# Optimization experiments

Measured on AMD Instinct MI355X. Metric: run time of the kernel, lower is better.

## Reference

```python
import jax, jax.numpy as jnp
import numpy as np

B, N, D = 8, 2048, 512
S = 4096  # max_swaps


def setup_inputs() -> dict:
    key = jax.random.key(0)
    ks = jax.random.split(key, 5)
    h = jax.random.normal(ks[0], (B, N, D), dtype=jnp.float32)
    indices = jax.random.randint(ks[1], (B, S, 4), 0, N, dtype=jnp.int64)
    # MLP params (Linear stores weight as (out,in) in torch; we keep (in,out) and matmul)
    W1 = jax.random.normal(ks[2], (4 * D, D), dtype=jnp.float32) * (1.0 / np.sqrt(4 * D))
    b1 = jnp.zeros((D,), dtype=jnp.float32)
    W2 = jax.random.normal(ks[3], (D, D // 2), dtype=jnp.float32) * (1.0 / np.sqrt(D))
    b2 = jnp.zeros((D // 2,), dtype=jnp.float32)
    W3 = jax.random.normal(ks[4], (D // 2, 1), dtype=jnp.float32) * (1.0 / np.sqrt(D // 2))
    b3 = jnp.zeros((1,), dtype=jnp.float32)
    return {"h": h, "indices": indices, "W1": W1, "b1": b1, "W2": W2, "b2": b2, "W3": W3, "b3": b3}


def reference(h, indices, W1, b1, W2, b2, W3, b3):
    # h: (B, N, D); indices: (B, S, 4) node ids per swap
    swap_emb = jnp.take_along_axis(h[:, None, :, :], indices[..., None].astype(jnp.int32),
                                   axis=2)  # broadcast-gather -> (B, S, 4, D)
    # equivalently: h[batch_idx, indices]; implemented as per-batch gather
    swap_emb = jax.vmap(lambda hb, ib: hb[ib])(h, indices)  # (B, S, 4, D)
    swap_feats = swap_emb.reshape(h.shape[0], indices.shape[1], -1)  # (B, S, 4D)
    x = jax.nn.gelu(swap_feats @ W1 + b1, approximate=False)
    x = jax.nn.gelu(x @ W2 + b2, approximate=False)
    scores = (x @ W3 + b3)[..., 0]  # (B, S)
    rates = jax.nn.softplus(scores)
    return rates
```

## Files before the change

### kernel.cpp

```cpp
#include <hip/hip_runtime.h>
#include <math.h>

#define BATCH 8
#define NNODES 2048
#define DDIM 512
#define SWAPS 4096
#define M_TOTAL (BATCH * SWAPS)
#define KD DDIM
#define K2 DDIM
#define N2 (DDIM / 2)

typedef __attribute__((ext_vector_type(8))) __bf16 bf16x8;
typedef __attribute__((ext_vector_type(4))) float f32x4;
typedef __attribute__((ext_vector_type(8))) unsigned short us8;
typedef unsigned short ushort_t;

__device__ __forceinline__ float gelu_fast(float x) {
    const float u = 0.7978845608028654f * x * fmaf(0.044715f * x, x, 1.0f);
    const float e = __expf(-2.0f * fabsf(u));
    float t = (1.0f - e) / (1.0f + e);
    t = copysignf(t, u);
    return 0.5f * x * (1.0f + t);
}
__device__ __forceinline__ float softplus_f(float x) {
    return fmaxf(x, 0.0f) + log1pf(expf(-fabsf(x)));
}
__device__ __forceinline__ unsigned short f2bf(float f) {
    unsigned int u = __builtin_bit_cast(unsigned int, f);
    u += 0x7FFFu + ((u >> 16) & 1u);
    return (unsigned short)(u >> 16);
}
__device__ __forceinline__ float bf2f(unsigned short s) {
    return __builtin_bit_cast(float, (unsigned int)s << 16);
}
__device__ __forceinline__ void glds16(const void* g, void* l) {
    __builtin_amdgcn_global_load_lds(
        (const __attribute__((address_space(1))) void*)g,
        (__attribute__((address_space(3))) void*)l, 16, 0, 0);
}

__global__ __launch_bounds__(256) void convert_kernel(
    const float* __restrict__ h, const float* __restrict__ W1,
    const float* __restrict__ W2, ushort_t* __restrict__ h_bf,
    ushort_t* __restrict__ W1pt, ushort_t* __restrict__ W2f)
{
    const int bid = blockIdx.x;
    if (bid < 8192) {
        size_t i = ((size_t)bid * 256 + threadIdx.x) * 4;
        float4 v = *(const float4*)(h + i);
        ushort4 o = { f2bf(v.x), f2bf(v.y), f2bf(v.z), f2bf(v.w) };
        *(ushort4*)(h_bf + i) = o;
    } else if (bid < 8192 + 1024) {
        size_t e = ((size_t)(bid - 8192) * 256 + threadIdx.x) * 4;
        const int k = (int)(e >> 9), n = (int)(e & 511);
        const int sg = k >> 9, d = k & 511;
        const int j = sg * 512 + n;
        float4 v = *(const float4*)(W1 + e);
        W1pt[(size_t)(j + 0) * KD + d] = f2bf(v.x);
        W1pt[(size_t)(j + 1) * KD + d] = f2bf(v.y);
        W1pt[(size_t)(j + 2) * KD + d] = f2bf(v.z);
        W1pt[(size_t)(j + 3) * KD + d] = f2bf(v.w);
    } else {
        size_t e = ((size_t)(bid - 9216) * 256 + threadIdx.x) * 4;
        const int k = (int)(e >> 8), n = (int)(e & 255);
        const int kc = k >> 5, quad = (k >> 3) & 3, pos = k & 7;
        const size_t base = (size_t)kc * 8192 + quad * 8 + pos;
        float4 v = *(const float4*)(W2 + e);
        W2f[base + (size_t)(n + 0) * 32] = f2bf(v.x);
        W2f[base + (size_t)(n + 1) * 32] = f2bf(v.y);
        W2f[base + (size_t)(n + 2) * 32] = f2bf(v.z);
        W2f[base + (size_t)(n + 3) * 32] = f2bf(v.w);
    }
}

__global__ __launch_bounds__(256) void gemm1_dense(
    const ushort_t* __restrict__ h_bf, const ushort_t* __restrict__ W1pt,
    ushort_t* __restrict__ P2)
{
    __shared__ __align__(16) char smem[32768];

    const int tid = threadIdx.x;
    const int w = tid >> 6, lane = tid & 63;
    const int quad = lane >> 4, l16 = lane & 15;
    const int wr = w >> 1, wc = w & 1;

    const int bid = blockIdx.x;
    const int xcd = bid & 7;
    const int r = bid >> 3;
    const int m0 = xcd * NNODES + (r & 15) * 128;
    const int n0 = (r >> 4) * 128;

    const int row0 = tid >> 2, sub = tid & 3;
    const int cg = (sub - (row0 >> 1)) & 3;
    const ushort_t* bA0 = h_bf + (size_t)(m0 + row0) * KD + cg * 8;
    const ushort_t* bA1 = h_bf + (size_t)(m0 + row0 + 64) * KD + cg * 8;
    const ushort_t* bB0 = W1pt + (size_t)(n0 + row0) * KD + cg * 8;
    const ushort_t* bB1 = W1pt + (size_t)(n0 + row0 + 64) * KD + cg * 8;

    int pa[4], pb[4];
    #pragma unroll
    for (int i = 0; i < 4; ++i) {
        const int rA = wr * 64 + i * 16 + l16;
        const int rB = wc * 64 + i * 16 + l16;
        pa[i] = rA * 64 + (((quad + (rA >> 1)) & 3) * 16);
        pb[i] = 8192 + rB * 64 + (((quad + (rB >> 1)) & 3) * 16);
    }

    f32x4 acc[4][4] = {};

    auto stage = [&](int kt, int half) {
        const int oo = kt * 32;
        char* base = smem + half * 16384;
        glds16(bA0 + oo, base + w * 1024);
        glds16(bA1 + oo, base + 4096 + w * 1024);
        glds16(bB0 + oo, base + 8192 + w * 1024);
        glds16(bB1 + oo, base + 12288 + w * 1024);
    };
    auto compute = [&](int half) {
        const char* base = smem + half * 16384;
        bf16x8 af[4], bfr[4];
        #pragma unroll
        for (int i = 0; i < 4; ++i) {
            af[i]  = *(const bf16x8*)(base + pa[i]);
            bfr[i] = *(const bf16x8*)(base + pb[i]);
        }
        #pragma unroll
        for (int i = 0; i < 4; ++i)
            #pragma unroll
            for (int jj = 0; jj < 4; ++jj)
                acc[i][jj] = __builtin_amdgcn_mfma_f32_16x16x32_bf16(
                    af[i], bfr[jj], acc[i][jj], 0, 0, 0);
    };

    for (int kt = 0; kt < 16; kt += 2) {
        stage(kt, 0);
        stage(kt + 1, 1);
        __syncthreads();
        compute(0);
        compute(1);
        __syncthreads();
    }

    #pragma unroll
    for (int jj = 0; jj < 4; ++jj) {
        const int j = n0 + wc * 64 + jj * 16 + l16;
        const int sg = j >> 9, nh = j & 511;
        const size_t base = ((size_t)(xcd * 2 + (nh >> 8)) * NNODES) * 1024
                          + (size_t)(sg << 8) + (nh & 255);
        #pragma unroll
        for (int i = 0; i < 4; ++i) {
            f32x4 v = acc[i][jj];
            #pragma unroll
            for (int rr = 0; rr < 4; ++rr) {
                const int node = (m0 + wr * 64 + i * 16 + quad * 4 + rr) & (NNODES - 1);
                P2[base + (size_t)node * 1024] = f2bf(v[rr]);
            }
        }
    }
}

__global__ __launch_bounds__(512) void fused_tail(
    const ushort_t* __restrict__ P2, const int* __restrict__ idx,
    const float* __restrict__ b1, const ushort_t* __restrict__ W2f,
    const float* __restrict__ b2, const float* __restrict__ W3,
    const float* __restrict__ b3, float* __restrict__ out)
{
    __shared__ __align__(16) char smem[66560];

    const int tid = threadIdx.x;
    const int w = tid >> 6, lane = tid & 63;
    const int quad = lane >> 4, l16 = lane & 15;

    const int bid = blockIdx.x;
    const int b = bid & 7;
    const int m0 = b * SWAPS + (bid >> 3) * 64;

    {
        const int row = tid >> 3;
        const int ws  = tid & 7;
        const int ap  = ws & 3;
        const int ncs = ws >> 2;
        const int acg = (ap - (row >> 1)) & 3;
        const int4 iv = *(const int4*)(idx + (size_t)(m0 + row) * 4);
        const ushort_t* Pr = P2 + (size_t)(b * 2 + ncs) * NNODES * 1024;
        const ushort_t* p0 = Pr + (size_t)iv.x * 1024 + 0 * 256;
        const ushort_t* p1 = Pr + (size_t)iv.y * 1024 + 1 * 256;
        const ushort_t* p2 = Pr + (size_t)iv.z * 1024 + 2 * 256;
        const ushort_t* p3 = Pr + (size_t)iv.w * 1024 + 3 * 256;
        #pragma unroll 4
        for (int it = 0; it < 8; ++it) {
            const int kc = ncs * 8 + it;
            const int pos0 = it * 32 + acg * 8;
            us8 v0 = *(const us8*)(p0 + pos0);
            us8 v1 = *(const us8*)(p1 + pos0);
            us8 v2 = *(const us8*)(p2 + pos0);
            us8 v3 = *(const us8*)(p3 + pos0);
            const float* bp = b1 + ncs * 256 + pos0;
            float4 ba = *(const float4*)bp;
            float4 bb = *(const float4*)(bp + 4);
            float s[8] = { ba.x, ba.y, ba.z, ba.w, bb.x, bb.y, bb.z, bb.w };
            #pragma unroll
            for (int e = 0; e < 8; ++e)
                s[e] += bf2f(v0[e]) + bf2f(v1[e]) + bf2f(v2[e]) + bf2f(v3[e]);
            us8 o;
            #pragma unroll
            for (int e = 0; e < 8; ++e) o[e] = f2bf(gelu_fast(s[e]));
            *(us8*)(smem + kc * 4096 + row * 64 + ap * 16) = o;
        }
    }
    __syncthreads();

    const int rg = w >> 2, cg = w & 3;
    int paRow[2];
    #pragma unroll
    for (int i = 0; i < 2; ++i) {
        const int rA = rg * 32 + i * 16 + l16;
        paRow[i] = rA * 64 + (((quad + (rA >> 1)) & 3) * 16);
    }
    const ushort_t* Bbase = W2f + (size_t)(cg * 64 + l16) * 32 + quad * 8;

    f32x4 acc[2][4] = {};

    #pragma unroll 2
    for (int kc = 0; kc < 16; ++kc) {
        bf16x8 af0 = *(const bf16x8*)(smem + kc * 4096 + paRow[0]);
        bf16x8 af1 = *(const bf16x8*)(smem + kc * 4096 + paRow[1]);
        #pragma unroll
        for (int jf = 0; jf < 4; ++jf) {
            bf16x8 bfr = *(const bf16x8*)(Bbase + (size_t)kc * 8192 + jf * 512);
            acc[0][jf] = __builtin_amdgcn_mfma_f32_16x16x32_bf16(af0, bfr, acc[0][jf], 0, 0, 0);
            acc[1][jf] = __builtin_amdgcn_mfma_f32_16x16x32_bf16(af1, bfr, acc[1][jf], 0, 0, 0);
        }
    }

    float part[2][4] = {};
    #pragma unroll
    for (int jf = 0; jf < 4; ++jf) {
        const int n = cg * 64 + jf * 16 + l16;
        const float w3 = W3[n];
        const float bb2 = b2[n];
        #pragma unroll
        for (int i = 0; i < 2; ++i) {
            f32x4 v = acc[i][jf];
            #pragma unroll
            for (int rr = 0; rr < 4; ++rr)
                part[i][rr] = fmaf(gelu_fast(v[rr] + bb2), w3, part[i][rr]);
        }
    }
    #pragma unroll
    for (int off = 1; off < 16; off <<= 1)
        #pragma unroll
        for (int i = 0; i < 2; ++i)
            #pragma unroll
            for (int rr = 0; rr < 4; ++rr)
                part[i][rr] += __shfl_xor(part[i][rr], off);

    float* red = (float*)(smem + 65536);
    if (l16 == 0) {
        #pragma unroll
        for (int i = 0; i < 2; ++i)
            #pragma unroll
            for (int rr = 0; rr < 4; ++rr)
                red[cg * 64 + rg * 32 + i * 16 + quad * 4 + rr] = part[i][rr];
    }
    __syncthreads();
    if (tid < 64) {
        const float v = red[tid] + red[64 + tid] + red[128 + tid] + red[192 + tid];
        out[m0 + tid] = softplus_f(v + b3[0]);
    }
}

extern "C" void kernel_launch(void* const* d_in, const int* in_sizes, int n_in,
                              void* d_out, int out_size, void* d_ws, size_t ws_size,
                              hipStream_t stream) {
    const float* h   = (const float*)d_in[0];
    const int*   idx = (const int*)d_in[1];
    const float* W1  = (const float*)d_in[2];
    const float* b1  = (const float*)d_in[3];
    const float* W2  = (const float*)d_in[4];
    const float* b2  = (const float*)d_in[5];
    const float* W3  = (const float*)d_in[6];
    const float* b3  = (const float*)d_in[7];
    float* out = (float*)d_out;

    char* ws = (char*)d_ws;
    ushort_t* P2    = (ushort_t*)ws;
    ushort_t* h_bf  = (ushort_t*)(ws + (64u << 20));
    ushort_t* W1pt  = (ushort_t*)(ws + (80u << 20));
    ushort_t* W2f   = (ushort_t*)(ws + (82u << 20));

    convert_kernel<<<9344, 256, 0, stream>>>(h, W1, W2, h_bf, W1pt, W2f);
    gemm1_dense<<<2048, 256, 0, stream>>>(h_bf, W1pt, P2);
    fused_tail<<<512, 512, 0, stream>>>(P2, idx, b1, W2f, b2, W3, b3, out);
}
```

Measured before the change: 179.2 us.

## Widen gemm1 tile to 128x256 and transpose W1 through LDS tiles

The dense gemm1 kernel now computes a 128x256 output tile per block instead of 128x128. Each wave holds 4x8 accumulators, and B fragments are reused across the four A rows, which halves the grid and cuts how often the h_bf tiles are reloaded. Separately, the W1 convert path now transposes through a padded shared-memory tile and writes 16-byte vectors instead of scattered 2-byte stores. The trade-off is more registers and LDS per block (48KB), which lowers occupancy, and fewer blocks (1024) to fill the GPU.

```diff
diff --git a/kernel.cpp b/kernel.cpp
--- a/kernel.cpp
+++ b/kernel.cpp
@@ -45,23 +45,40 @@
     ushort_t* __restrict__ W1pt, ushort_t* __restrict__ W2f)
 {
     const int bid = blockIdx.x;
+    const int tid = threadIdx.x;
     if (bid < 8192) {
-        size_t i = ((size_t)bid * 256 + threadIdx.x) * 4;
+        size_t i = ((size_t)bid * 256 + tid) * 4;
         float4 v = *(const float4*)(h + i);
         ushort4 o = { f2bf(v.x), f2bf(v.y), f2bf(v.z), f2bf(v.w) };
         *(ushort4*)(h_bf + i) = o;
-    } else if (bid < 8192 + 1024) {
-        size_t e = ((size_t)(bid - 8192) * 256 + threadIdx.x) * 4;
-        const int k = (int)(e >> 9), n = (int)(e & 511);
-        const int sg = k >> 9, d = k & 511;
-        const int j = sg * 512 + n;
-        float4 v = *(const float4*)(W1 + e);
-        W1pt[(size_t)(j + 0) * KD + d] = f2bf(v.x);
-        W1pt[(size_t)(j + 1) * KD + d] = f2bf(v.y);
-        W1pt[(size_t)(j + 2) * KD + d] = f2bf(v.z);
-        W1pt[(size_t)(j + 3) * KD + d] = f2bf(v.w);
+    } else if (bid < 8192 + 256) {
+        __shared__ ushort_t sT[64][72];
+        const int tb = bid - 8192;
+        const int kt = tb >> 3, nt = tb & 7;
+        const int kl = tid >> 4;
+        const int n4 = (tid & 15) * 4;
+        #pragma unroll
+        for (int p = 0; p < 4; ++p) {
+            const int k_local = p * 16 + kl;
+            float4 v = *(const float4*)(W1 + (size_t)(kt * 64 + k_local) * 512
+                                        + nt * 64 + n4);
+            sT[n4 + 0][k_local] = f2bf(v.x);
+            sT[n4 + 1][k_local] = f2bf(v.y);
+            sT[n4 + 2][k_local] = f2bf(v.z);
+            sT[n4 + 3][k_local] = f2bf(v.w);
+        }
+        __syncthreads();
+        const int n_local = tid >> 2, ch = tid & 3;
+        const int j = (kt >> 3) * 512 + nt * 64 + n_local;
+        const int d0 = (kt & 7) * 64 + ch * 16;
+        us8 o0, o1;
+        #pragma unroll
+        for (int e = 0; e < 8; ++e) { o0[e] = sT[n_local][ch * 16 + e];
+                                      o1[e] = sT[n_local][ch * 16 + 8 + e]; }
+        *(us8*)(W1pt + (size_t)j * KD + d0)     = o0;
+        *(us8*)(W1pt + (size_t)j * KD + d0 + 8) = o1;
     } else {
-        size_t e = ((size_t)(bid - 9216) * 256 + threadIdx.x) * 4;
+        size_t e = ((size_t)(bid - 8448) * 256 + tid) * 4;
         const int k = (int)(e >> 8), n = (int)(e & 255);
         const int kc = k >> 5, quad = (k >> 3) & 3, pos = k & 7;
         const size_t base = (size_t)kc * 8192 + quad * 8 + pos;
@@ -77,7 +94,7 @@
     const ushort_t* __restrict__ h_bf, const ushort_t* __restrict__ W1pt,
     ushort_t* __restrict__ P2)
 {
-    __shared__ __align__(16) char smem[32768];
+    __shared__ __align__(16) char smem[49152];
 
     const int tid = threadIdx.x;
     const int w = tid >> 6, lane = tid & 63;
@@ -88,48 +105,54 @@
     const int xcd = bid & 7;
     const int r = bid >> 3;
     const int m0 = xcd * NNODES + (r & 15) * 128;
-    const int n0 = (r >> 4) * 128;
+    const int n0 = (r >> 4) * 256;
 
     const int row0 = tid >> 2, sub = tid & 3;
     const int cg = (sub - (row0 >> 1)) & 3;
     const ushort_t* bA0 = h_bf + (size_t)(m0 + row0) * KD + cg * 8;
     const ushort_t* bA1 = h_bf + (size_t)(m0 + row0 + 64) * KD + cg * 8;
-    const ushort_t* bB0 = W1pt + (size_t)(n0 + row0) * KD + cg * 8;
-    const ushort_t* bB1 = W1pt + (size_t)(n0 + row0 + 64) * KD + cg * 8;
-
-    int pa[4], pb[4];
+    const ushort_t* bB[4];
+    #pragma unroll
+    for (int g = 0; g < 4; ++g)
+        bB[g] = W1pt + (size_t)(n0 + g * 64 + row0) * KD + cg * 8;
+
+    int pa[4], pb[8];
     #pragma unroll
     for (int i = 0; i < 4; ++i) {
         const int rA = wr * 64 + i * 16 + l16;
-        const int rB = wc * 64 + i * 16 + l16;
         pa[i] = rA * 64 + (((quad + (rA >> 1)) & 3) * 16);
-        pb[i] = 8192 + rB * 64 + (((quad + (rB >> 1)) & 3) * 16);
-    }
-
-    f32x4 acc[4][4] = {};
+    }
+    #pragma unroll
+    for (int jf = 0; jf < 8; ++jf) {
+        const int rB = wc * 128 + jf * 16 + l16;
+        pb[jf] = 8192 + rB * 64 + (((quad + (rB >> 1)) & 3) * 16);
+    }
+
+    f32x4 acc[4][8] = {};
 
     auto stage = [&](int kt, int half) {
         const int oo = kt * 32;
-        char* base = smem + half * 16384;
+        char* base = smem + half * 24576;
         glds16(bA0 + oo, base + w * 1024);
         glds16(bA1 + oo, base + 4096 + w * 1024);
-        glds16(bB0 + oo, base + 8192 + w * 1024);
-        glds16(bB1 + oo, base + 12288 + w * 1024);
+        #pragma unroll
+        for (int g = 0; g < 4; ++g)
+            glds16(bB[g] + oo, base + 8192 + g * 4096 + w * 1024);
     };
     auto compute = [&](int half) {
-        const char* base = smem + half * 16384;
-        bf16x8 af[4], bfr[4];
+        const char* base = smem + half * 24576;
+        bf16x8 bfr[8];
+        #pragma unroll
+        for (int jf = 0; jf < 8; ++jf)
+            bfr[jf] = *(const bf16x8*)(base + pb[jf]);
         #pragma unroll
         for (int i = 0; i < 4; ++i) {
-            af[i]  = *(const bf16x8*)(base + pa[i]);
-            bfr[i] = *(const bf16x8*)(base + pb[i]);
-        }
-        #pragma unroll
-        for (int i = 0; i < 4; ++i)
-            #pragma unroll
-            for (int jj = 0; jj < 4; ++jj)
-                acc[i][jj] = __builtin_amdgcn_mfma_f32_16x16x32_bf16(
-                    af[i], bfr[jj], acc[i][jj], 0, 0, 0);
+            bf16x8 af = *(const bf16x8*)(base + pa[i]);
+            #pragma unroll
+            for (int jf = 0; jf < 8; ++jf)
+                acc[i][jf] = __builtin_amdgcn_mfma_f32_16x16x32_bf16(
+                    af, bfr[jf], acc[i][jf], 0, 0, 0);
+        }
     };
 
     for (int kt = 0; kt < 16; kt += 2) {
@@ -142,14 +165,14 @@
     }
 
     #pragma unroll
-    for (int jj = 0; jj < 4; ++jj) {
-        const int j = n0 + wc * 64 + jj * 16 + l16;
+    for (int jf = 0; jf < 8; ++jf) {
+        const int j = n0 + wc * 128 + jf * 16 + l16;
         const int sg = j >> 9, nh = j & 511;
         const size_t base = ((size_t)(xcd * 2 + (nh >> 8)) * NNODES) * 1024
                           + (size_t)(sg << 8) + (nh & 255);
         #pragma unroll
         for (int i = 0; i < 4; ++i) {
-            f32x4 v = acc[i][jj];
+            f32x4 v = acc[i][jf];
             #pragma unroll
             for (int rr = 0; rr < 4; ++rr) {
                 const int node = (m0 + wr * 64 + i * 16 + quad * 4 + rr) & (NNODES - 1);
@@ -289,7 +312,7 @@
     ushort_t* W1pt  = (ushort_t*)(ws + (80u << 20));
     ushort_t* W2f   = (ushort_t*)(ws + (82u << 20));
 
-    convert_kernel<<<9344, 256, 0, stream>>>(h, W1, W2, h_bf, W1pt, W2f);
-    gemm1_dense<<<2048, 256, 0, stream>>>(h_bf, W1pt, P2);
+    convert_kernel<<<8576, 256, 0, stream>>>(h, W1, W2, h_bf, W1pt, W2f);
+    gemm1_dense<<<1024, 256, 0, stream>>>(h_bf, W1pt, P2);
     fused_tail<<<512, 512, 0, stream>>>(P2, idx, b1, W2f, b2, W3, b3, out);
 }
```

Result: slower. 205.7 us (+14.8%).
